# Kernel optimization log

Measured on AMD Instinct MI355X. Metric: run time of the kernel, lower is better.

Reference implementation:

```python
import jax, jax.numpy as jnp
import numpy as np

HIDDEN = 1024
NUM_HEADS = 16
HEAD_DIM = HIDDEN // NUM_HEADS
EPS = 1e-05


def setup_inputs() -> dict:
    key = jax.random.key(0)
    ks = jax.random.split(key, 6)
    B, S = 4, 2048
    x = jax.random.normal(ks[0], (B, S, HIDDEN), dtype=jnp.float32)
    # trunc_normal_(std=0.02) approximated by scaled normal
    w_in = jax.random.normal(ks[1], (3 * HIDDEN, HIDDEN), dtype=jnp.float32) * 0.02
    b_in = jax.random.normal(ks[2], (3 * HIDDEN,), dtype=jnp.float32) * 0.02
    w_norm = jnp.ones((HIDDEN,), dtype=jnp.float32)
    lim = 1.0 / np.sqrt(HIDDEN)
    w_out = jax.random.uniform(ks[3], (HIDDEN, HIDDEN), dtype=jnp.float32, minval=-lim, maxval=lim)
    b_out = jax.random.uniform(ks[4], (HIDDEN,), dtype=jnp.float32, minval=-lim, maxval=lim)
    return {"x": x, "w_in": w_in, "b_in": b_in, "w_norm": w_norm, "w_out": w_out, "b_out": b_out}


def _rms_norm(x, w, eps):
    var = jnp.mean(jnp.square(x), axis=-1, keepdims=True)
    return x * jax.lax.rsqrt(var + eps) * w


def reference(x, w_in, b_in, w_norm, w_out, b_out):
    B, S, _ = x.shape
    xn = _rms_norm(x, w_norm, EPS)
    qkv = jnp.einsum('bsd,ed->bse', xn, w_in) + b_in  # [B,S,3*HIDDEN]
    q, k, v = jnp.split(qkv, 3, axis=-1)
    # [B,S,H*D] -> [B,H,S,D]
    def split_heads(t):
        return t.reshape(B, S, NUM_HEADS, HEAD_DIM).transpose(0, 2, 1, 3)
    q, k, v = split_heads(q), split_heads(k), split_heads(v)
    scale = 1.0 / np.sqrt(HEAD_DIM)
    scores = jnp.einsum('bhqd,bhkd->bhqk', q, k) * scale
    attn = jax.nn.softmax(scores, axis=-1)
    o = jnp.einsum('bhqk,bhkd->bhqd', attn, v)
    o = o.transpose(0, 2, 1, 3).reshape(B, S, HIDDEN)
    return jnp.einsum('bsd,ed->bse', o, w_out) + b_out
```

## Files before the change

kernel.cpp:

```cpp
#include <hip/hip_runtime.h>
#include <stdint.h>

typedef short bf16x4 __attribute__((ext_vector_type(4)));
typedef short bf16x8 __attribute__((ext_vector_type(8)));
typedef _Float16 f16x8 __attribute__((ext_vector_type(8)));
typedef float f32x4 __attribute__((ext_vector_type(4)));
typedef float f32x16 __attribute__((ext_vector_type(16)));
typedef unsigned int u32x4 __attribute__((ext_vector_type(4)));
typedef unsigned int u32x2 __attribute__((ext_vector_type(2)));

#if __has_builtin(__builtin_amdgcn_exp2f)
#define EXP2 __builtin_amdgcn_exp2f
#else
#define EXP2 exp2f
#endif

__device__ __forceinline__ short f2bf(float f) {
  union { float f; uint32_t u; } v; v.f = f;
  uint32_t r = (v.u + 0x7fffu + ((v.u >> 16) & 1u)) >> 16;
  return (short)(uint16_t)r;
}

__device__ __forceinline__ unsigned cvtpk_bf16(float lo, float hi) {
  unsigned r;
  asm("v_cvt_pk_bf16_f32 %0, %1, %2" : "=v"(r) : "v"(lo), "v"(hi));
  return r;
}

#if __has_builtin(__builtin_amdgcn_permlane32_swap)
__device__ __forceinline__ void plane32_swap(unsigned& a, unsigned& b) {
  u32x2 r = __builtin_amdgcn_permlane32_swap(a, b, false, false);
  a = r[0]; b = r[1];
}
__device__ __forceinline__ float xhalf_max(float x) {
  unsigned xu = __builtin_bit_cast(unsigned, x);
  u32x2 r = __builtin_amdgcn_permlane32_swap(xu, xu, false, false);
  return fmaxf(__builtin_bit_cast(float, r[0]), __builtin_bit_cast(float, r[1]));
}
__device__ __forceinline__ float xhalf_sum(float x) {
  unsigned xu = __builtin_bit_cast(unsigned, x);
  u32x2 r = __builtin_amdgcn_permlane32_swap(xu, xu, false, false);
  return __builtin_bit_cast(float, r[0]) + __builtin_bit_cast(float, r[1]);
}
#else
__device__ __forceinline__ void plane32_swap(unsigned& a, unsigned& b) {
  asm("s_nop 1\n\tv_permlane32_swap_b32 %0, %1" : "+v"(a), "+v"(b));
}
__device__ __forceinline__ float xhalf_max(float x) { return fmaxf(x, __shfl_xor(x, 32, 64)); }
__device__ __forceinline__ float xhalf_sum(float x) { return x + __shfl_xor(x, 32, 64); }
#endif

__device__ __forceinline__ float fmax3(float a, float b, float c) {
  return fmaxf(fmaxf(a, b), c);
}

__device__ __forceinline__ float tmax16(const f32x16& s) {
  float a0 = fmax3(s[0], s[1], s[2]);
  float a1 = fmax3(s[3], s[4], s[5]);
  float a2 = fmax3(s[6], s[7], s[8]);
  float a3 = fmax3(s[9], s[10], s[11]);
  float a4 = fmax3(s[12], s[13], s[14]);
  float b0 = fmax3(a0, a1, s[15]);
  float b1 = fmax3(a2, a3, a4);
  return fmaxf(b0, b1);
}
__device__ __forceinline__ float tsum16(const f32x16& s) {
  float a0 = (s[0] + s[1]) + (s[2] + s[3]);
  float a1 = (s[4] + s[5]) + (s[6] + s[7]);
  float a2 = (s[8] + s[9]) + (s[10] + s[11]);
  float a3 = (s[12] + s[13]) + (s[14] + s[15]);
  return (a0 + a1) + (a2 + a3);
}

__device__ __forceinline__ f32x16 zero16() {
  f32x16 z;
#pragma unroll
  for (int i = 0; i < 16; ++i) z[i] = 0.f;
  return z;
}

__device__ __forceinline__ void gld_lds16(const void* g, void* l) {
  __builtin_amdgcn_global_load_lds(
      (__attribute__((address_space(1))) const void*)g,
      (__attribute__((address_space(3))) void*)l, 16, 0, 0);
}

__global__ __launch_bounds__(256) void k_rmsnorm(const float* __restrict__ x,
                                                 const float* __restrict__ wn,
                                                 short* __restrict__ xn) {
  const int row = blockIdx.x;
  const int t = threadIdx.x;
  const float4 v = reinterpret_cast<const float4*>(x + (size_t)row * 1024)[t];
  float ss = v.x * v.x + v.y * v.y + v.z * v.z + v.w * v.w;
#pragma unroll
  for (int m = 32; m >= 1; m >>= 1) ss += __shfl_xor(ss, m, 64);
  __shared__ float red[4];
  if ((t & 63) == 0) red[t >> 6] = ss;
  __syncthreads();
  const float tot = red[0] + red[1] + red[2] + red[3];
  const float rr = rsqrtf(tot * (1.0f / 1024.0f) + 1e-5f);
  const float4 g = reinterpret_cast<const float4*>(wn)[t];
  bf16x4 o;
  o[0] = f2bf(v.x * rr * g.x);
  o[1] = f2bf(v.y * rr * g.y);
  o[2] = f2bf(v.z * rr * g.z);
  o[3] = f2bf(v.w * rr * g.w);
  reinterpret_cast<bf16x4*>(xn + (size_t)row * 1024)[t] = o;
}

__global__ __launch_bounds__(256) void k_cast_bf(const float* __restrict__ in,
                                                 short* __restrict__ out, int n4) {
  int i = blockIdx.x * 256 + threadIdx.x;
  if (i >= n4) return;
  float4 v = reinterpret_cast<const float4*>(in)[i];
  bf16x4 o;
  o[0] = f2bf(v.x); o[1] = f2bf(v.y); o[2] = f2bf(v.z); o[3] = f2bf(v.w);
  reinterpret_cast<bf16x4*>(out)[i] = o;
}

__global__ __launch_bounds__(256) void k_cast_f16(const float* __restrict__ in,
                                                  _Float16* __restrict__ out, int n4) {
  int i = blockIdx.x * 256 + threadIdx.x;
  if (i >= n4) return;
  float4 v = reinterpret_cast<const float4*>(in)[i];
  _Float16 o[4] = {(_Float16)v.x, (_Float16)v.y, (_Float16)v.z, (_Float16)v.w};
  reinterpret_cast<ulong1*>(out)[i] = *reinterpret_cast<ulong1*>(o);
}

__global__ __launch_bounds__(256) void k_gemm_qkv(const short* __restrict__ A,
                                                  const short* __restrict__ B,
                                                  const float* __restrict__ bias,
                                                  short* __restrict__ qb,
                                                  short* __restrict__ kb,
                                                  short* __restrict__ vb) {
  __shared__ __align__(16) short As[128 * 32];
  __shared__ __align__(16) short Bs[128 * 32];
  const int t = threadIdx.x;
  const int orig = blockIdx.y * 24 + blockIdx.x;
  const int swz = (orig & 7) * 192 + (orig >> 3);
  const long bn0 = (long)(swz % 24) * 128;
  const long bm0 = (long)(swz / 24) * 128;
  const int w = t >> 6, l = t & 63;
  const int wr = (w >> 1) * 64, wc = (w & 1) * 64;
  const int lm = l & 15, h = l >> 4;
  f32x4 acc[4][4];
#pragma unroll
  for (int i = 0; i < 4; ++i)
#pragma unroll
    for (int j = 0; j < 4; ++j) acc[i][j] = (f32x4){0.f, 0.f, 0.f, 0.f};
  const int srow = t >> 2, scol = (t & 3) * 8;
  const short* Ag = A + (bm0 + srow) * 1024 + scol;
  const short* Bg = B + (bn0 + srow) * 1024 + scol;
  short* AsP = As + t * 8;
  short* BsP = Bs + t * 8;
  for (int kt = 0; kt < 32; ++kt) {
    const int k0 = kt << 5;
    gld_lds16(Ag + k0, AsP);
    gld_lds16(Ag + k0 + 64 * 1024, AsP + 2048);
    gld_lds16(Bg + k0, BsP);
    gld_lds16(Bg + k0 + 64 * 1024, BsP + 2048);
    __syncthreads();
    bf16x8 af[4], bfr[4];
#pragma unroll
    for (int mi = 0; mi < 4; ++mi)
      af[mi] = *reinterpret_cast<const bf16x8*>(As + (wr + mi * 16 + lm) * 32 + h * 8);
#pragma unroll
    for (int ni = 0; ni < 4; ++ni)
      bfr[ni] = *reinterpret_cast<const bf16x8*>(Bs + (wc + ni * 16 + lm) * 32 + h * 8);
    __builtin_amdgcn_s_setprio(1);
#pragma unroll
    for (int mi = 0; mi < 4; ++mi)
#pragma unroll
      for (int ni = 0; ni < 4; ++ni)
        acc[mi][ni] = __builtin_amdgcn_mfma_f32_16x16x32_bf16(af[mi], bfr[ni], acc[mi][ni], 0, 0, 0);
    __builtin_amdgcn_s_setprio(0);
    __syncthreads();
  }
#pragma unroll
  for (int ni = 0; ni < 4; ++ni) {
    const int ncol = (int)bn0 + wc + ni * 16 + lm;
    const float bv = bias[ncol];
    const int which = ncol >> 10;
    const int e = ncol & 1023;
#pragma unroll
    for (int mi = 0; mi < 4; ++mi) {
#pragma unroll
      for (int r = 0; r < 4; ++r) {
        const long mrow = bm0 + wr + mi * 16 + h * 4 + r;
        const float val = acc[mi][ni][r] + bv;
        const long off = (((mrow >> 11) * 16 + (e >> 6)) * 2048 + (mrow & 2047)) * 64 + (e & 63);
        if (which == 0) qb[off] = f2bf(val * 0.18033688011112042f);
        else if (which == 1) kb[off] = f2bf(val);
        else vb[off] = f2bf(val);
      }
    }
  }
}

__global__ __launch_bounds__(256) void k_gemm_out(const _Float16* __restrict__ A,
                                                  const _Float16* __restrict__ B,
                                                  const float* __restrict__ bias,
                                                  float* __restrict__ outp) {
  __shared__ __align__(16) _Float16 As[128 * 32];
  __shared__ __align__(16) _Float16 Bs[128 * 32];
  const int t = threadIdx.x;
  const int orig = blockIdx.y * 8 + blockIdx.x;
  const int swz = (orig & 7) * 64 + (orig >> 3);
  const long bn0 = (long)(swz % 8) * 128;
  const long bm0 = (long)(swz / 8) * 128;
  const int w = t >> 6, l = t & 63;
  const int wr = (w >> 1) * 64, wc = (w & 1) * 64;
  const int lm = l & 15, h = l >> 4;
  f32x4 acc[4][4];
#pragma unroll
  for (int i = 0; i < 4; ++i)
#pragma unroll
    for (int j = 0; j < 4; ++j) acc[i][j] = (f32x4){0.f, 0.f, 0.f, 0.f};
  const int srow = t >> 2, scol = (t & 3) * 8;
  const _Float16* Ag = A + (bm0 + srow) * 1024 + scol;
  const _Float16* Bg = B + (bn0 + srow) * 1024 + scol;
  _Float16* AsP = As + t * 8;
  _Float16* BsP = Bs + t * 8;
  for (int kt = 0; kt < 32; ++kt) {
    const int k0 = kt << 5;
    gld_lds16(Ag + k0, AsP);
    gld_lds16(Ag + k0 + 64 * 1024, AsP + 2048);
    gld_lds16(Bg + k0, BsP);
    gld_lds16(Bg + k0 + 64 * 1024, BsP + 2048);
    __syncthreads();
    f16x8 af[4], bfr[4];
#pragma unroll
    for (int mi = 0; mi < 4; ++mi)
      af[mi] = *reinterpret_cast<const f16x8*>(As + (wr + mi * 16 + lm) * 32 + h * 8);
#pragma unroll
    for (int ni = 0; ni < 4; ++ni)
      bfr[ni] = *reinterpret_cast<const f16x8*>(Bs + (wc + ni * 16 + lm) * 32 + h * 8);
    __builtin_amdgcn_s_setprio(1);
#pragma unroll
    for (int mi = 0; mi < 4; ++mi)
#pragma unroll
      for (int ni = 0; ni < 4; ++ni)
        acc[mi][ni] = __builtin_amdgcn_mfma_f32_16x16x32_f16(af[mi], bfr[ni], acc[mi][ni], 0, 0, 0);
    __builtin_amdgcn_s_setprio(0);
    __syncthreads();
  }
#pragma unroll
  for (int ni = 0; ni < 4; ++ni) {
    const int ncol = (int)bn0 + wc + ni * 16 + lm;
    const float bv = bias[ncol];
#pragma unroll
    for (int mi = 0; mi < 4; ++mi) {
#pragma unroll
      for (int r = 0; r < 4; ++r) {
        const long mrow = bm0 + wr + mi * 16 + h * 4 + r;
        outp[mrow * 1024 + ncol] = acc[mi][ni][r] + bv;
      }
    }
  }
}

__global__ __launch_bounds__(256) void k_transpose_v(const short* __restrict__ v,
                                                     short* __restrict__ vt) {
  __shared__ short tile[64][72];
  const int bh = blockIdx.y, st = blockIdx.x;
  const int t = threadIdx.x;
  const int r = t >> 2, c0 = (t & 3) * 16;
  const short* src = v + ((size_t)(bh * 2048 + st * 64 + r)) * 64 + c0;
  bf16x8 a = *reinterpret_cast<const bf16x8*>(src);
  bf16x8 b = *reinterpret_cast<const bf16x8*>(src + 8);
#pragma unroll
  for (int j = 0; j < 8; ++j) tile[r][c0 + j] = a[j];
#pragma unroll
  for (int j = 0; j < 8; ++j) tile[r][c0 + 8 + j] = b[j];
  __syncthreads();
  __align__(16) short tmp[16];
#pragma unroll
  for (int j = 0; j < 16; ++j) tmp[j] = tile[c0 + j][r];
  short* dst = vt + ((size_t)(bh * 64 + r)) * 2048 + st * 64 + c0;
  *reinterpret_cast<bf16x8*>(dst) = *reinterpret_cast<const bf16x8*>(tmp);
  *reinterpret_cast<bf16x8*>(dst + 8) = *reinterpret_cast<const bf16x8*>(tmp + 8);
}

__global__ __launch_bounds__(256, 2) void k_attn(const short* __restrict__ q,
                                                 const short* __restrict__ k,
                                                 const short* __restrict__ vt,
                                                 _Float16* __restrict__ o) {
  __shared__ __align__(16) short Ks[2][2048];
  __shared__ __align__(16) short Vs[2][2048];
  const int bh = blockIdx.y;
  const int qt = blockIdx.x;
  const int t = threadIdx.x;
  const int w = t >> 6, l = t & 63;
  const int lq = l & 31, hh = l >> 5;
  const int xr = lq & 7;
  const int qbase = qt * 256 + w * 64;

  bf16x8 qf[2][4];
#pragma unroll
  for (int qh = 0; qh < 2; ++qh) {
    const short* qp = q + ((size_t)(bh * 2048 + qbase + qh * 32 + lq)) * 64 + hh * 8;
#pragma unroll
    for (int db = 0; db < 4; ++db)
      qf[qh][db] = *reinterpret_cast<const bf16x8*>(qp + db * 16);
  }

  const int gg = t;
  const int uK = gg ^ ((gg >> 3) & 7);
  const int vrow = gg >> 2;
  const int vcol = (gg & 3) ^ (vrow & 3);
  const short* kh = k + (size_t)bh * 2048 * 64;
  const short* vh = vt + (size_t)bh * 64 * 2048;
  const short* ksrc = kh + uK * 8;
  const short* vsrc = vh + vrow * 2048 + vcol * 8;

  int koff[4], voff[2][2];
#pragma unroll
  for (int db = 0; db < 4; ++db)
    koff[db] = (lq * 8 + ((db * 2 + hh) ^ xr)) * 8;
#pragma unroll
  for (int dt = 0; dt < 2; ++dt)
#pragma unroll
    for (int kg = 0; kg < 2; ++kg)
      voff[dt][kg] = ((dt * 32 + lq) * 4 + ((kg * 2 + hh) ^ (lq & 3))) * 8;

  f32x16 oa00 = zero16(), oa01 = zero16();
  f32x16 oa10 = zero16(), oa11 = zero16();
  float mr0 = -1e30f, mr1 = -1e30f, lr0 = 0.f, lr1 = 0.f;

  gld_lds16(ksrc, &Ks[0][gg * 8]);
  gld_lds16(vsrc, &Vs[0][gg * 8]);
  __syncthreads();

  int cur = 0;
  for (int kt = 0; kt < 64; ++kt) {
    const int kn = (kt + 1) & 63;
    const int nb = cur ^ 1;
    gld_lds16(ksrc + kn * 2048, &Ks[nb][gg * 8]);
    gld_lds16(vsrc + kn * 32, &Vs[nb][gg * 8]);

    const short* kb_ = Ks[cur];
    const short* vb_ = Vs[cur];
    f32x16 s0 = zero16(), s1 = zero16();
    __builtin_amdgcn_s_setprio(1);
#pragma unroll
    for (int db = 0; db < 4; ++db) {
      bf16x8 kf = *reinterpret_cast<const bf16x8*>(kb_ + koff[db]);
      s0 = __builtin_amdgcn_mfma_f32_32x32x16_bf16(kf, qf[0][db], s0, 0, 0, 0);
      s1 = __builtin_amdgcn_mfma_f32_32x32x16_bf16(kf, qf[1][db], s1, 0, 0, 0);
    }
    __builtin_amdgcn_s_setprio(0);
    float tm0 = xhalf_max(tmax16(s0));
    float tm1 = xhalf_max(tmax16(s1));
    if (!__all((tm0 <= mr0 + 8.f) && (tm1 <= mr1 + 8.f))) {
      const float mn0 = fmaxf(mr0, tm0), mn1 = fmaxf(mr1, tm1);
      const float c0 = EXP2(mr0 - mn0), c1 = EXP2(mr1 - mn1);
      lr0 *= c0; lr1 *= c1;
#pragma unroll
      for (int r = 0; r < 16; ++r) {
        oa00[r] *= c0; oa01[r] *= c0;
        oa10[r] *= c1; oa11[r] *= c1;
      }
      mr0 = mn0; mr1 = mn1;
    }
#pragma unroll
    for (int r = 0; r < 16; ++r) {
      s0[r] = EXP2(s0[r] - mr0);
      s1[r] = EXP2(s1[r] - mr1);
    }
    lr0 += tsum16(s0);
    lr1 += tsum16(s1);
    __builtin_amdgcn_s_setprio(1);
#pragma unroll
    for (int kg = 0; kg < 2; ++kg) {
      const int b0 = kg * 8;
      unsigned p00 = cvtpk_bf16(s0[b0 + 0], s0[b0 + 1]);
      unsigned p01 = cvtpk_bf16(s0[b0 + 2], s0[b0 + 3]);
      unsigned p02 = cvtpk_bf16(s0[b0 + 4], s0[b0 + 5]);
      unsigned p03 = cvtpk_bf16(s0[b0 + 6], s0[b0 + 7]);
      plane32_swap(p00, p02);
      plane32_swap(p01, p03);
      u32x4 pw0 = {p00, p01, p02, p03};
      bf16x8 pf0 = *reinterpret_cast<bf16x8*>(&pw0);
      unsigned p10 = cvtpk_bf16(s1[b0 + 0], s1[b0 + 1]);
      unsigned p11 = cvtpk_bf16(s1[b0 + 2], s1[b0 + 3]);
      unsigned p12 = cvtpk_bf16(s1[b0 + 4], s1[b0 + 5]);
      unsigned p13 = cvtpk_bf16(s1[b0 + 6], s1[b0 + 7]);
      plane32_swap(p10, p12);
      plane32_swap(p11, p13);
      u32x4 pw1 = {p10, p11, p12, p13};
      bf16x8 pf1 = *reinterpret_cast<bf16x8*>(&pw1);
      bf16x8 vf0 = *reinterpret_cast<const bf16x8*>(vb_ + voff[0][kg]);
      oa00 = __builtin_amdgcn_mfma_f32_32x32x16_bf16(vf0, pf0, oa00, 0, 0, 0);
      oa10 = __builtin_amdgcn_mfma_f32_32x32x16_bf16(vf0, pf1, oa10, 0, 0, 0);
      bf16x8 vf1 = *reinterpret_cast<const bf16x8*>(vb_ + voff[1][kg]);
      oa01 = __builtin_amdgcn_mfma_f32_32x32x16_bf16(vf1, pf0, oa01, 0, 0, 0);
      oa11 = __builtin_amdgcn_mfma_f32_32x32x16_bf16(vf1, pf1, oa11, 0, 0, 0);
    }
    __builtin_amdgcn_s_setprio(0);
    __syncthreads();
    cur = nb;
  }
  const float inv0 = 1.0f / xhalf_sum(lr0);
  const float inv1 = 1.0f / xhalf_sum(lr1);
  const int b = bh >> 4, hd = bh & 15;
  _Float16* ob0 = o + ((size_t)(b * 2048 + qbase + lq)) * 1024 + hd * 64;
  _Float16* ob1 = ob0 + 32 * 1024;
#pragma unroll
  for (int r2 = 0; r2 < 16; ++r2) {
    const int d0 = (r2 & 3) + 8 * (r2 >> 2) + 4 * hh;
    ob0[d0] = (_Float16)(oa00[r2] * inv0);
    ob0[d0 + 32] = (_Float16)(oa01[r2] * inv0);
    ob1[d0] = (_Float16)(oa10[r2] * inv1);
    ob1[d0 + 32] = (_Float16)(oa11[r2] * inv1);
  }
}

extern "C" void kernel_launch(void* const* d_in, const int* in_sizes, int n_in,
                              void* d_out, int out_size, void* d_ws, size_t ws_size,
                              hipStream_t stream) {
  const float* x = (const float*)d_in[0];
  const float* w_in = (const float*)d_in[1];
  const float* b_in = (const float*)d_in[2];
  const float* w_norm = (const float*)d_in[3];
  const float* w_out = (const float*)d_in[4];
  const float* b_out = (const float*)d_in[5];
  float* out = (float*)d_out;
  char* ws = (char*)d_ws;
  short* xn = (short*)(ws);
  short* win_b = (short*)(ws + 16777216);
  _Float16* wout_h = (_Float16*)(ws + 23068672);
  short* qb = (short*)(ws + 25165824);
  short* kb = (short*)(ws + 41943040);
  short* vb = (short*)(ws + 58720256);
  short* vt = (short*)(ws + 75497472);
  _Float16* ob = (_Float16*)vb;

  k_cast_bf<<<3072, 256, 0, stream>>>(w_in, win_b, 786432);
  k_cast_f16<<<1024, 256, 0, stream>>>(w_out, wout_h, 262144);
  k_rmsnorm<<<8192, 256, 0, stream>>>(x, w_norm, xn);
  k_gemm_qkv<<<dim3(24, 64), 256, 0, stream>>>(xn, win_b, b_in, qb, kb, vb);
  k_transpose_v<<<dim3(32, 64), 256, 0, stream>>>(vb, vt);
  k_attn<<<dim3(8, 64), 256, 0, stream>>>(qb, kb, vt, ob);
  k_gemm_out<<<dim3(8, 64), 256, 0, stream>>>(ob, wout_h, b_out, out);
}
```

Before: 231.5 us.

## Deepen attention K/V prefetch to four-stage ring with one barrier and swizzle block order

The attention kernel's K/V LDS staging goes from double buffering to a 4-slot ring, keeping three tiles in flight. A manual vmcnt wait plus a single barrier per iteration replaces the end-of-loop __syncthreads. The block index is also remapped so consecutive launched blocks cover different heads/q-tiles, changing cache locality across CUs. LDS use doubles to 32KB per block, which may limit occupancy. The vmcnt(4) value assumes exactly two global loads per stage, and tail iterations reload tile 63 redundantly.

```diff
diff --git a/kernel.cpp b/kernel.cpp
--- a/kernel.cpp
+++ b/kernel.cpp
@@ -285,10 +285,12 @@
                                                  const short* __restrict__ k,
                                                  const short* __restrict__ vt,
                                                  _Float16* __restrict__ o) {
-  __shared__ __align__(16) short Ks[2][2048];
-  __shared__ __align__(16) short Vs[2][2048];
-  const int bh = blockIdx.y;
-  const int qt = blockIdx.x;
+  __shared__ __align__(16) short Ks[4][2048];
+  __shared__ __align__(16) short Vs[4][2048];
+  const int orig = blockIdx.y * 8 + blockIdx.x;
+  const int work = (orig & 7) * 64 + (orig >> 3);
+  const int bh = work >> 3;
+  const int qt = work & 7;
   const int t = threadIdx.x;
   const int w = t >> 6, l = t & 63;
   const int lq = l & 31, hh = l >> 5;
@@ -327,19 +329,21 @@
   f32x16 oa10 = zero16(), oa11 = zero16();
   float mr0 = -1e30f, mr1 = -1e30f, lr0 = 0.f, lr1 = 0.f;
 
-  gld_lds16(ksrc, &Ks[0][gg * 8]);
-  gld_lds16(vsrc, &Vs[0][gg * 8]);
-  __syncthreads();
-
-  int cur = 0;
+#pragma unroll
+  for (int p = 0; p < 3; ++p) {
+    gld_lds16(ksrc + p * 2048, &Ks[p][gg * 8]);
+    gld_lds16(vsrc + p * 32, &Vs[p][gg * 8]);
+  }
+
   for (int kt = 0; kt < 64; ++kt) {
-    const int kn = (kt + 1) & 63;
-    const int nb = cur ^ 1;
-    gld_lds16(ksrc + kn * 2048, &Ks[nb][gg * 8]);
-    gld_lds16(vsrc + kn * 32, &Vs[nb][gg * 8]);
-
-    const short* kb_ = Ks[cur];
-    const short* vb_ = Vs[cur];
+    asm volatile("s_waitcnt vmcnt(4)" ::: "memory");
+    __builtin_amdgcn_s_barrier();
+    int kn = kt + 3; if (kn > 63) kn = 63;
+    gld_lds16(ksrc + kn * 2048, &Ks[(kt + 3) & 3][gg * 8]);
+    gld_lds16(vsrc + kn * 32, &Vs[(kt + 3) & 3][gg * 8]);
+
+    const short* kb_ = Ks[kt & 3];
+    const short* vb_ = Vs[kt & 3];
     f32x16 s0 = zero16(), s1 = zero16();
     __builtin_amdgcn_s_setprio(1);
 #pragma unroll
@@ -397,8 +401,6 @@
       oa11 = __builtin_amdgcn_mfma_f32_32x32x16_bf16(vf1, pf1, oa11, 0, 0, 0);
     }
     __builtin_amdgcn_s_setprio(0);
-    __syncthreads();
-    cur = nb;
   }
   const float inv0 = 1.0f / xhalf_sum(lr0);
   const float inv1 = 1.0f / xhalf_sum(lr1);
```

After: 227.4 us. About the same (-1.8%).
